# Kernel tuning notes

Hardware: AMD Instinct MI355X
Metric: run time of the kernel (lower is better)

The kernel has to match this reference:

```python
import jax, jax.numpy as jnp
import numpy as np

B, C, K, F = 16, 64, 128, 6
HORIZON_S = 3.0  # conflict_horizon_s default
EPS = 1e-06


def setup_inputs() -> dict:
    rng = np.random.default_rng(0)
    # base adjacency: sparse random directed graph, zero diagonal
    A = (rng.random((B, K, K)) < 0.05).astype(np.float32)
    A[:, np.arange(K), np.arange(K)] = 0.0
    # candidates: exactly one unordered-pair edit (state in {0:none,1:i->j,2:j->i})
    cand = np.repeat(A[:, None], C, axis=1).copy()
    i = rng.integers(0, K - 1, (B, C))
    j = i + 1 + (rng.integers(0, K - 1, (B, C)) % (K - 1 - i))
    state = rng.integers(0, 3, (B, C))
    bidx = np.arange(B)[:, None] * np.ones((1, C), dtype=np.int64)
    cidx = np.ones((B, 1), dtype=np.int64) * np.arange(C)[None, :]
    cand[bidx, cidx, i, j] = (state == 1).astype(np.float32)
    cand[bidx, cidx, j, i] = (state == 2).astype(np.float32)
    cand[:, 0] = A  # candidate 0 is NOOP (keep A_t)
    # agent features: (x, y, yaw, vx, vy, pad)
    feat = rng.normal(size=(B, K, F)).astype(np.float32)
    feat[..., 0:2] *= 20.0  # spread positions over ~40m
    mask = (rng.random((B, K)) > 0.1).astype(np.float32)
    return {
        "A_t": jnp.asarray(A),
        "candidate_A": jnp.asarray(cand),
        "agent_feat": jnp.asarray(feat),
        "agent_mask": jnp.asarray(mask),
    }


def _edit_tokens(A_t, candidate_A):
    # vectorized version of EBSTM.extract_edit_tokens
    Bn, Cn, Kn, _ = candidate_A.shape
    base = A_t > 0.5                      # [B,K,K]
    cb = candidate_A > 0.5                # [B,C,K,K]
    diff = cb != base[:, None]            # [B,C,K,K]
    upper = jnp.triu(jnp.ones((Kn, Kn), dtype=bool), k=1)
    pairdiff = (diff | jnp.swapaxes(diff, -1, -2)) & upper
    flat = pairdiff.reshape(Bn, Cn, Kn * Kn)
    changed = flat.any(-1)                # [B,C]
    idx = jnp.argmax(flat, axis=-1)       # first changed pair in row-major (i,j) order
    i = idx // Kn
    j = idx % Kn
    barange = jnp.arange(Bn)[:, None]
    carange = jnp.arange(Cn)[None, :]
    b_ij = base[barange, i, j]
    b_ji = base[barange, j, i]
    c_ij = cb[barange, carange, i, j]
    c_ji = cb[barange, carange, j, i]
    prev = jnp.where(b_ij & ~b_ji, 1, jnp.where(b_ji & ~b_ij, 2, 0))
    nxt = jnp.where(c_ij & ~c_ji, 1, jnp.where(c_ji & ~c_ij, 2, 0))
    tokens = jnp.stack([i, j, prev, nxt], axis=-1).astype(jnp.int32)
    return tokens * changed[..., None].astype(jnp.int32)


def _relation_state3(cb):
    # cb: bool [B,C,K,K]
    at = jnp.swapaxes(cb, -1, -2)
    return ((cb & ~at).astype(jnp.int32) * 1
            + (~cb & at).astype(jnp.int32) * 2
            + (cb & at).astype(jnp.int32) * 3)


def _batched_acyclic(cb, agent_mask):
    # vectorized Kahn zero-indegree peel, matching EBSTM._is_acyclic semantics:
    #  - indegree counts edges from ALL sources (valid or not)
    #  - only valid nodes are ever removed
    #  - special case: <=1 valid node is acyclic
    Bn, Cn, Kn, _ = cb.shape
    valid = (agent_mask > 0.5)[:, None, :]           # [B,1,K]
    Ai = cb.astype(jnp.int32)                        # [B,C,K,K]
    indeg = Ai.sum(axis=-2) * valid.astype(jnp.int32)  # [B,C,K]
    removed = jnp.zeros((Bn, Cn, Kn), dtype=bool)

    def body(t, carry):
        indeg, removed = carry
        rem = valid & (~removed) & (indeg == 0)
        dec = jnp.einsum('bci,bcij->bcj', rem.astype(jnp.int32), Ai)
        return indeg - dec, removed | rem

    indeg, removed = jax.lax.fori_loop(0, Kn, body, (indeg, removed))
    vcount = valid.astype(jnp.int32).sum(-1)          # [B,1]
    return (removed.astype(jnp.int32).sum(-1) == vcount) | (vcount <= 1)


def _pair_dists(agent_feat):
    pos = agent_feat[..., 0:2]
    vel = agent_feat[..., 3:5]
    # _pair_distance: d[b,i,j] = |pos_i - pos_j|
    d = jnp.linalg.norm(pos[:, :, None] - pos[:, None, :], axis=-1)
    # _pair_closest_approach_distance: r[b,i,j] = pos_j - pos_i
    r = pos[:, None, :] - pos[:, :, None]
    v = vel[:, None, :] - vel[:, :, None]
    vv = (v * v).sum(-1)
    rv = (r * v).sum(-1)
    t_star = jnp.clip(-rv / (vv + EPS), 0.0, HORIZON_S)
    dmin = jnp.linalg.norm(r + v * t_star[..., None], axis=-1)
    eye = jnp.eye(dmin.shape[-1], dtype=bool)[None]
    dmin = jnp.where(eye, jnp.inf, dmin)
    return jnp.stack([d, dmin], axis=0)  # [2,B,K,K]


def reference(A_t, candidate_A, agent_feat, agent_mask):
    cb = candidate_A > 0.5
    tokens = _edit_tokens(A_t, candidate_A)          # [B,C,4] int32
    rel = _relation_state3(cb)                       # [B,C,K,K] int32
    acyclic = _batched_acyclic(cb, agent_mask)       # [B,C] bool
    dists = _pair_dists(agent_feat)                  # [2,B,K,K] float32
    return tokens, rel, acyclic, dists
```

## Files before the change

### kernel.cpp

```cpp
#include <hip/hip_runtime.h>
#include <cstdint>
#include <math.h>

#define KN 128
#define BATCH 16
#define CAND 64

static constexpr size_t TOK_OFF = 0;
static constexpr size_t REL_OFF = (size_t)BATCH * CAND * 4;
static constexpr size_t ACY_OFF = REL_OFF + (size_t)BATCH * CAND * KN * KN;
static constexpr size_t DST_OFF = ACY_OFF + (size_t)BATCH * CAND;

#define DIAG_BIG 1.0e30f

__global__ __launch_bounds__(256) void base_bits_kernel(const float* __restrict__ A_t,
                                                        uint32_t* __restrict__ bits) {
    int tid  = blockIdx.x * 256 + threadIdx.x;
    int wave = tid >> 6;
    int lane = tid & 63;
    int half = wave & 1;
    int row  = wave >> 1;
    float v = A_t[(size_t)row * KN + half * 64 + lane];
    unsigned long long m = __ballot(v > 0.5f);
    if (lane == 0) {
        bits[row * 4 + half * 2]     = (uint32_t)m;
        bits[row * 4 + half * 2 + 1] = (uint32_t)(m >> 32);
    }
}

__global__ __launch_bounds__(256) void main_kernel(const float* __restrict__ cand,
                                                   const float* __restrict__ mask,
                                                   const uint32_t* __restrict__ baseBits,
                                                   float* __restrict__ out) {
    __shared__ uint32_t adj[KN][5];
    __shared__ uint32_t baseB[KN][4];
    __shared__ int      indeg[KN];
    __shared__ uint32_t validW[4];
    __shared__ uint32_t remW[4];
    __shared__ uint32_t removedW[4];
    __shared__ int      minIdx;

    const int t    = threadIdx.x;
    const int lane = t & 63;
    const int wave = t >> 6;
    const int bc   = blockIdx.x;
    const int b    = bc >> 6;

    const float* cptr = cand + (size_t)bc * (KN * KN);

    if (t == 0) minIdx = 0x7fffffff;
    if (t < 4)  removedW[t] = 0;

    for (int w = t; w < 512; w += 256) {
        baseB[w >> 2][w & 3] = baseBits[b * 512 + w];
    }

    if (wave < 2) {
        float mv = mask[b * KN + wave * 64 + lane];
        unsigned long long m = __ballot(mv > 0.5f);
        if (lane == 0) {
            validW[wave * 2]     = (uint32_t)m;
            validW[wave * 2 + 1] = (uint32_t)(m >> 32);
        }
    }

    for (int m = 0; m < 16; ++m) {
        int rowPair = m * 4 + wave;
        int r   = rowPair * 2 + (lane >> 5);
        int sub = lane & 31;
        const float4 v = ((const float4*)(cptr + (size_t)r * KN))[sub];
        uint32_t nib = (v.x > 0.5f ? 1u : 0u) | (v.y > 0.5f ? 2u : 0u) |
                       (v.z > 0.5f ? 4u : 0u) | (v.w > 0.5f ? 8u : 0u);
        uint32_t word = nib << (4 * (sub & 7));
        word |= __shfl_xor(word, 1);
        word |= __shfl_xor(word, 2);
        word |= __shfl_xor(word, 4);
        if ((lane & 7) == 0) adj[r][sub >> 3] = word;
    }
    __syncthreads();

    {
        float* relp = out + REL_OFF + (size_t)bc * (KN * KN);
        for (int m = 0; m < 16; ++m) {
            int q  = t + 256 * m;
            int i  = q >> 5;
            int j0 = (q & 31) * 4;
            uint32_t wij = adj[i][j0 >> 5];
            int sh = j0 & 31;
            uint32_t iw = i >> 5, ib = i & 31;
            uint32_t t0 = (adj[j0 + 0][iw] >> ib) & 1u;
            uint32_t t1 = (adj[j0 + 1][iw] >> ib) & 1u;
            uint32_t t2 = (adj[j0 + 2][iw] >> ib) & 1u;
            uint32_t t3 = (adj[j0 + 3][iw] >> ib) & 1u;
            float4 o;
            o.x = (float)(((wij >> (sh + 0)) & 1u) + 2u * t0);
            o.y = (float)(((wij >> (sh + 1)) & 1u) + 2u * t1);
            o.z = (float)(((wij >> (sh + 2)) & 1u) + 2u * t2);
            o.w = (float)(((wij >> (sh + 3)) & 1u) + 2u * t3);
            ((float4*)relp)[q] = o;
        }
    }

    for (int idx = t; idx < 512; idx += 256) {
        int i = idx >> 2, k = idx & 3;
        uint32_t diff = adj[i][k] ^ baseB[i][k];
        if (diff) {
            int base = k * 32;
            uint32_t up, low;
            if (i < base)            { up = diff; low = 0u; }
            else if (i >= base + 31) { up = 0u; low = (i > base + 31) ? diff : (diff & 0x7fffffffu); }
            else {
                int s = i - base;
                up  = diff & (0xffffffffu << (s + 1));
                low = diff & ((1u << s) - 1u);
            }
            int c1 = 0x7fffffff, c2 = 0x7fffffff;
            if (up)  c1 = (i << 7) | (base + __builtin_ctz(up));
            if (low) { int cc = base + __builtin_ctz(low); c2 = (cc << 7) | i; }
            int cm = min(c1, c2);
            if (cm != 0x7fffffff) atomicMin(&minIdx, cm);
        }
    }

    if (t < KN) {
        uint32_t jw = t >> 5, jb = t & 31;
        int s = 0;
        for (int i = 0; i < KN; ++i) s += (adj[i][jw] >> jb) & 1u;
        bool valid = (validW[jw] >> jb) & 1u;
        indeg[t] = valid ? s : 0;
    }
    __syncthreads();

    if (t == 0) {
        float* tok = out + TOK_OFF + (size_t)bc * 4;
        int mi = minIdx;
        if (mi != 0x7fffffff) {
            int i = mi >> 7, j = mi & 127;
            uint32_t b_ij = (baseB[i][j >> 5] >> (j & 31)) & 1u;
            uint32_t b_ji = (baseB[j][i >> 5] >> (i & 31)) & 1u;
            uint32_t c_ij = (adj[i][j >> 5] >> (j & 31)) & 1u;
            uint32_t c_ji = (adj[j][i >> 5] >> (i & 31)) & 1u;
            int prev = (b_ij && !b_ji) ? 1 : ((b_ji && !b_ij) ? 2 : 0);
            int nxt  = (c_ij && !c_ji) ? 1 : ((c_ji && !c_ij) ? 2 : 0);
            tok[0] = (float)i; tok[1] = (float)j; tok[2] = (float)prev; tok[3] = (float)nxt;
        } else {
            tok[0] = 0.f; tok[1] = 0.f; tok[2] = 0.f; tok[3] = 0.f;
        }
    }

    for (int it = 0; it < KN; ++it) {
        bool rem = false;
        if (t < KN) {
            uint32_t jw = t >> 5, jb = t & 31;
            bool valid   = (validW[jw] >> jb) & 1u;
            bool removed = (removedW[jw] >> jb) & 1u;
            rem = valid && !removed && (indeg[t] == 0);
        }
        unsigned long long m = __ballot(rem);
        if (wave < 2 && lane == 0) {
            remW[wave * 2]     = (uint32_t)m;
            remW[wave * 2 + 1] = (uint32_t)(m >> 32);
        }
        __syncthreads();
        uint32_t r0 = remW[0], r1 = remW[1], r2 = remW[2], r3 = remW[3];
        if ((r0 | r1 | r2 | r3) == 0u) break;
        if (t < 4) removedW[t] |= remW[t];
        if (t < KN) {
            uint32_t jw = t >> 5, jb = t & 31;
            int dec = 0;
            uint32_t rw[4] = {r0, r1, r2, r3};
            for (int w = 0; w < 4; ++w) {
                uint32_t mm = rw[w];
                while (mm) {
                    int i = w * 32 + __builtin_ctz(mm);
                    mm &= mm - 1;
                    dec += (adj[i][jw] >> jb) & 1u;
                }
            }
            indeg[t] -= dec;
        }
        __syncthreads();
    }
    __syncthreads();

    if (t == 0) {
        int rc = __popc(removedW[0]) + __popc(removedW[1]) + __popc(removedW[2]) + __popc(removedW[3]);
        int vc = __popc(validW[0]) + __popc(validW[1]) + __popc(validW[2]) + __popc(validW[3]);
        out[ACY_OFF + bc] = ((rc == vc) || (vc <= 1)) ? 1.0f : 0.0f;
    }
}

__global__ __launch_bounds__(128) void dists_kernel(const float* __restrict__ feat,
                                                    float* __restrict__ out) {
    int bi = blockIdx.x;
    int b = bi >> 7, i = bi & 127;
    int j = threadIdx.x;
    const float* fi = feat + (size_t)bi * 6;
    const float* fj = feat + (size_t)(b * KN + j) * 6;
    float pix = fi[0], piy = fi[1], vix = fi[3], viy = fi[4];
    float pjx = fj[0], pjy = fj[1], vjx = fj[3], vjy = fj[4];
    float dx = pix - pjx, dy = piy - pjy;
    float d = sqrtf(dx * dx + dy * dy);
    float rx = pjx - pix, ry = pjy - piy;
    float vx = vjx - vix, vy = vjy - viy;
    float vv = vx * vx + vy * vy;
    float rv = rx * vx + ry * vy;
    float ts = fminf(fmaxf(-rv / (vv + 1e-6f), 0.0f), 3.0f);
    float mx = rx + vx * ts, my = ry + vy * ts;
    float dmin = (i == j) ? DIAG_BIG : sqrtf(mx * mx + my * my);
    float* o = out + DST_OFF;
    o[(size_t)(b * KN + i) * KN + j] = d;
    o[(size_t)((BATCH + b) * KN + i) * KN + j] = dmin;
}

extern "C" void kernel_launch(void* const* d_in, const int* in_sizes, int n_in,
                              void* d_out, int out_size, void* d_ws, size_t ws_size,
                              hipStream_t stream) {
    const float* A_t  = (const float*)d_in[0];
    const float* cand = (const float*)d_in[1];
    const float* feat = (const float*)d_in[2];
    const float* mask = (const float*)d_in[3];
    float* out = (float*)d_out;
    uint32_t* bits = (uint32_t*)d_ws;

    base_bits_kernel<<<1024, 256, 0, stream>>>(A_t, bits);
    main_kernel<<<BATCH * CAND, 256, 0, stream>>>(cand, mask, bits, out);
    dists_kernel<<<BATCH * KN, 128, 0, stream>>>(feat, out);
}
```

Baseline: 134.0 us.

## Fuse base-bits, main and distance kernels into one launch with nontemporal I/O

Merges the three kernels into a single kernel. Each block now packs the base adjacency bits for its batch directly from A_t and also computes two rows of the pair-distance output (1024 blocks × 2 rows = 16×128 rows). Candidate loads and rel/dist stores use nontemporal builtins to avoid polluting cache with streamed data. This removes two launches and the workspace round trip, at the cost of each block redundantly re-reading its batch's A_t (64× per batch) and doing extra work per block.

New measurement: 137.7 us. +2.7%, slower.

```diff
diff --git a/kernel.cpp b/kernel.cpp
--- a/kernel.cpp
+++ b/kernel.cpp
@@ -5,6 +5,8 @@
 #define KN 128
 #define BATCH 16
 #define CAND 64
+
+typedef float vfloat4 __attribute__((ext_vector_type(4)));
 
 static constexpr size_t TOK_OFF = 0;
 static constexpr size_t REL_OFF = (size_t)BATCH * CAND * 4;
@@ -13,25 +15,11 @@
 
 #define DIAG_BIG 1.0e30f
 
-__global__ __launch_bounds__(256) void base_bits_kernel(const float* __restrict__ A_t,
-                                                        uint32_t* __restrict__ bits) {
-    int tid  = blockIdx.x * 256 + threadIdx.x;
-    int wave = tid >> 6;
-    int lane = tid & 63;
-    int half = wave & 1;
-    int row  = wave >> 1;
-    float v = A_t[(size_t)row * KN + half * 64 + lane];
-    unsigned long long m = __ballot(v > 0.5f);
-    if (lane == 0) {
-        bits[row * 4 + half * 2]     = (uint32_t)m;
-        bits[row * 4 + half * 2 + 1] = (uint32_t)(m >> 32);
-    }
-}
-
-__global__ __launch_bounds__(256) void main_kernel(const float* __restrict__ cand,
-                                                   const float* __restrict__ mask,
-                                                   const uint32_t* __restrict__ baseBits,
-                                                   float* __restrict__ out) {
+__global__ __launch_bounds__(256) void fused_kernel(const float* __restrict__ A_t,
+                                                    const float* __restrict__ cand,
+                                                    const float* __restrict__ feat,
+                                                    const float* __restrict__ mask,
+                                                    float* __restrict__ out) {
     __shared__ uint32_t adj[KN][5];
     __shared__ uint32_t baseB[KN][4];
     __shared__ int      indeg[KN];
@@ -47,13 +35,10 @@
     const int b    = bc >> 6;
 
     const float* cptr = cand + (size_t)bc * (KN * KN);
+    const float* aptr = A_t + (size_t)b * (KN * KN);
 
     if (t == 0) minIdx = 0x7fffffff;
     if (t < 4)  removedW[t] = 0;
-
-    for (int w = t; w < 512; w += 256) {
-        baseB[w >> 2][w & 3] = baseBits[b * 512 + w];
-    }
 
     if (wave < 2) {
         float mv = mask[b * KN + wave * 64 + lane];
@@ -68,7 +53,21 @@
         int rowPair = m * 4 + wave;
         int r   = rowPair * 2 + (lane >> 5);
         int sub = lane & 31;
-        const float4 v = ((const float4*)(cptr + (size_t)r * KN))[sub];
+        const float4 v = ((const float4*)(aptr + (size_t)r * KN))[sub];
+        uint32_t nib = (v.x > 0.5f ? 1u : 0u) | (v.y > 0.5f ? 2u : 0u) |
+                       (v.z > 0.5f ? 4u : 0u) | (v.w > 0.5f ? 8u : 0u);
+        uint32_t word = nib << (4 * (sub & 7));
+        word |= __shfl_xor(word, 1);
+        word |= __shfl_xor(word, 2);
+        word |= __shfl_xor(word, 4);
+        if ((lane & 7) == 0) baseB[r][sub >> 3] = word;
+    }
+
+    for (int m = 0; m < 16; ++m) {
+        int rowPair = m * 4 + wave;
+        int r   = rowPair * 2 + (lane >> 5);
+        int sub = lane & 31;
+        vfloat4 v = __builtin_nontemporal_load(((const vfloat4*)(cptr + (size_t)r * KN)) + sub);
         uint32_t nib = (v.x > 0.5f ? 1u : 0u) | (v.y > 0.5f ? 2u : 0u) |
                        (v.z > 0.5f ? 4u : 0u) | (v.w > 0.5f ? 8u : 0u);
         uint32_t word = nib << (4 * (sub & 7));
@@ -76,6 +75,27 @@
         word |= __shfl_xor(word, 2);
         word |= __shfl_xor(word, 4);
         if ((lane & 7) == 0) adj[r][sub >> 3] = word;
+    }
+
+    {
+        int bi = 2 * bc + (t >> 7);
+        int b2 = bi >> 7, i = bi & 127, j = t & 127;
+        const float* fi = feat + (size_t)bi * 6;
+        const float* fj = feat + (size_t)(b2 * KN + j) * 6;
+        float pix = fi[0], piy = fi[1], vix = fi[3], viy = fi[4];
+        float pjx = fj[0], pjy = fj[1], vjx = fj[3], vjy = fj[4];
+        float dx = pix - pjx, dy = piy - pjy;
+        float d = sqrtf(dx * dx + dy * dy);
+        float rx = pjx - pix, ry = pjy - piy;
+        float vx = vjx - vix, vy = vjy - viy;
+        float vv = vx * vx + vy * vy;
+        float rv = rx * vx + ry * vy;
+        float ts = fminf(fmaxf(-rv / (vv + 1e-6f), 0.0f), 3.0f);
+        float mx = rx + vx * ts, my = ry + vy * ts;
+        float dmin = (i == j) ? DIAG_BIG : sqrtf(mx * mx + my * my);
+        float* o = out + DST_OFF;
+        __builtin_nontemporal_store(d,    o + (size_t)(b2 * KN + i) * KN + j);
+        __builtin_nontemporal_store(dmin, o + (size_t)((BATCH + b2) * KN + i) * KN + j);
     }
     __syncthreads();
 
@@ -92,12 +112,12 @@
             uint32_t t1 = (adj[j0 + 1][iw] >> ib) & 1u;
             uint32_t t2 = (adj[j0 + 2][iw] >> ib) & 1u;
             uint32_t t3 = (adj[j0 + 3][iw] >> ib) & 1u;
-            float4 o;
+            vfloat4 o;
             o.x = (float)(((wij >> (sh + 0)) & 1u) + 2u * t0);
             o.y = (float)(((wij >> (sh + 1)) & 1u) + 2u * t1);
             o.z = (float)(((wij >> (sh + 2)) & 1u) + 2u * t2);
             o.w = (float)(((wij >> (sh + 3)) & 1u) + 2u * t3);
-            ((float4*)relp)[q] = o;
+            __builtin_nontemporal_store(o, ((vfloat4*)relp) + q);
         }
     }
 
@@ -190,29 +210,6 @@
     }
 }
 
-__global__ __launch_bounds__(128) void dists_kernel(const float* __restrict__ feat,
-                                                    float* __restrict__ out) {
-    int bi = blockIdx.x;
-    int b = bi >> 7, i = bi & 127;
-    int j = threadIdx.x;
-    const float* fi = feat + (size_t)bi * 6;
-    const float* fj = feat + (size_t)(b * KN + j) * 6;
-    float pix = fi[0], piy = fi[1], vix = fi[3], viy = fi[4];
-    float pjx = fj[0], pjy = fj[1], vjx = fj[3], vjy = fj[4];
-    float dx = pix - pjx, dy = piy - pjy;
-    float d = sqrtf(dx * dx + dy * dy);
-    float rx = pjx - pix, ry = pjy - piy;
-    float vx = vjx - vix, vy = vjy - viy;
-    float vv = vx * vx + vy * vy;
-    float rv = rx * vx + ry * vy;
-    float ts = fminf(fmaxf(-rv / (vv + 1e-6f), 0.0f), 3.0f);
-    float mx = rx + vx * ts, my = ry + vy * ts;
-    float dmin = (i == j) ? DIAG_BIG : sqrtf(mx * mx + my * my);
-    float* o = out + DST_OFF;
-    o[(size_t)(b * KN + i) * KN + j] = d;
-    o[(size_t)((BATCH + b) * KN + i) * KN + j] = dmin;
-}
-
 extern "C" void kernel_launch(void* const* d_in, const int* in_sizes, int n_in,
                               void* d_out, int out_size, void* d_ws, size_t ws_size,
                               hipStream_t stream) {
@@ -221,9 +218,6 @@
     const float* feat = (const float*)d_in[2];
     const float* mask = (const float*)d_in[3];
     float* out = (float*)d_out;
-    uint32_t* bits = (uint32_t*)d_ws;
-
-    base_bits_kernel<<<1024, 256, 0, stream>>>(A_t, bits);
-    main_kernel<<<BATCH * CAND, 256, 0, stream>>>(cand, mask, bits, out);
-    dists_kernel<<<BATCH * KN, 128, 0, stream>>>(feat, out);
+
+    fused_kernel<<<BATCH * CAND, 256, 0, stream>>>(A_t, cand, feat, mask, out);
 }
```
